# Optimization experiments

Hardware: AMD Instinct MI355X
Metric: run time of the kernel (lower is better)

Reference implementation:

```python
import jax, jax.numpy as jnp
import numpy as np

EPS = 1e-8
N_CLASSES = 11


def _instance_loss(views_1, views_2, masks, labels):
    # views_*: [1, C, H, W]; masks: [1, K, H, W] binary; labels: [1, K] in [0,11)
    C = views_1.shape[1]
    X1 = views_1[0].reshape(C, -1)                      # [C, P]
    X2 = views_2[0].reshape(C, -1)                      # [C, P]
    K = masks.shape[1]
    M = (masks[0].reshape(K, -1) == 1).astype(X1.dtype) # [K, P]
    lab = labels[0]                                     # [K]

    counts = M.sum(axis=1)                              # [K] pixels per instance
    cnt = jnp.maximum(counts, 1.0)

    # per-instance mean feature vector over masked view-1 pixels
    per_chan_sum = M @ X1.T                             # [K, C]
    means = per_chan_sum / cnt[:, None]                 # [K, C]

    # torch.std over ALL elements of the gathered [N_k, C] block (unbiased)
    n_elem = counts * C                                 # [K]
    sum_all = per_chan_sum.sum(axis=1)                  # [K]
    mean_all = sum_all / jnp.maximum(n_elem, 1.0)
    sumsq = M @ (X1 * X1).sum(axis=0)                   # [K]
    var = (sumsq - n_elem * mean_all * mean_all) / jnp.maximum(n_elem - 1.0, 1.0)
    std = jnp.sqrt(jnp.maximum(var, 0.0))               # [K]

    # pairwise mean cosine sim: sim[i,j] = mean_{p in mask_j} cos(means[i], X2[:,p])
    norm_m = jnp.sqrt((means * means).sum(axis=1))      # [K]
    norm_2 = jnp.sqrt((X2 * X2).sum(axis=0))            # [P]
    D = means @ X2                                      # [K, P]
    ratio = D / jnp.maximum(norm_m[:, None] * norm_2[None, :], EPS)
    sim = (ratio @ M.T) / cnt[None, :]                  # [K, K]

    same = lab[:, None] == lab[None, :]
    eye = jnp.eye(K, dtype=bool)

    instance_sim = jnp.zeros(N_CLASSES, X1.dtype).at[lab].add(jnp.diagonal(sim))
    class_sim = jnp.zeros(N_CLASSES, X1.dtype).at[lab].add(
        jnp.where(same & ~eye, sim, 0.0).sum(axis=1))
    class_std = jnp.zeros(N_CLASSES, X1.dtype).at[lab].add(std)

    # negative-pair buckets: human={1,2}, 4wheel={3..8}, 2wheel={9,10}
    g_hum_4w = (lab >= 1) & (lab <= 8)                  # human or 4wheel
    g_4w_2w = (lab >= 3) & (lab <= 10)                  # 4wheel or 2wheel
    g_hum_2w = ((lab >= 1) & (lab <= 2)) | ((lab >= 9) & (lab <= 10))
    diff = ~same

    def neg_bucket(g):
        pair = diff & g[:, None] & g[None, :]
        c = pair.sum().astype(X1.dtype)
        s = jnp.where(pair, sim, 0.0).sum()
        return jnp.where(c > 1, s / c, s).reshape(1)

    neg_4w_hum = neg_bucket(g_hum_4w)
    neg_4w_2w = neg_bucket(g_4w_2w)
    neg_hum_2w = neg_bucket(g_hum_2w)

    class_counts = jnp.zeros(N_CLASSES, X1.dtype).at[lab].add(1.0)
    many = class_counts > 1
    instance_sim = jnp.where(many, instance_sim / jnp.maximum(class_counts, 1.0), instance_sim)
    class_sim = jnp.where(
        many, class_sim / jnp.maximum(class_counts * (class_counts - 1.0), 1.0), class_sim)
    class_std = jnp.where(many, class_std / jnp.maximum(class_counts, 1.0), class_std)

    return instance_sim, class_sim, neg_4w_hum, neg_4w_2w, neg_hum_2w, class_std


def setup_inputs() -> dict:
    key = jax.random.key(0)
    k1, k2, k3, k4 = jax.random.split(key, 4)
    views_1 = jax.random.normal(k1, (1, 64, 512, 512), dtype=jnp.float32)
    views_2 = jax.random.normal(k2, (1, 64, 512, 512), dtype=jnp.float32)
    masks = jax.random.randint(k3, (1, 16, 512, 512), 0, 2, dtype=jnp.int32)
    labels = jax.random.randint(k4, (1, 16), 0, 11, dtype=jnp.int32)
    return {"views_1": views_1, "views_2": views_2, "masks": masks, "labels": labels}


def reference(views_1, views_2, masks, labels):
    return _instance_loss(views_1, views_2, masks, labels)
```

## Files before the change

kernel.cpp:

```cpp
#include <hip/hip_runtime.h>

#define PIX 262144
#define CCH 64
#define KK  16

typedef __attribute__((ext_vector_type(8))) short short8;
typedef __attribute__((ext_vector_type(4))) float f32x4;

__device__ __forceinline__ unsigned short f2bf(float f) {
    unsigned u = __float_as_uint(f);
    return (unsigned short)((u + 0x7FFFu + ((u >> 16) & 1u)) >> 16);
}
__device__ __forceinline__ float bf2f(unsigned short h) {
    return __uint_as_float(((unsigned)h) << 16);
}

__global__ __launch_bounds__(256) void k1a_pack(
        const int* __restrict__ masks, unsigned short* __restrict__ packed,
        float* __restrict__ counts_s) {
    int t = blockIdx.x * 256 + threadIdx.x;
    int p = t * 2;
    unsigned m0 = 0, m1 = 0;
    #pragma unroll
    for (int k = 0; k < KK; ++k) {
        int2 mv = *(const int2*)(masks + (size_t)k * PIX + p);
        m0 |= (unsigned)(mv.x == 1) << k;
        m1 |= (unsigned)(mv.y == 1) << k;
    }
    packed[p]     = (unsigned short)m0;
    packed[p + 1] = (unsigned short)m1;

    __shared__ float wc[4][16];
    int wid = threadIdx.x >> 6, lane = threadIdx.x & 63;
    #pragma unroll
    for (int k = 0; k < KK; ++k) {
        unsigned long long b0 = __ballot((m0 >> k) & 1u);
        unsigned long long b1 = __ballot((m1 >> k) & 1u);
        if (lane == 0) wc[wid][k] = (float)(__popcll(b0) + __popcll(b1));
    }
    __syncthreads();
    if (threadIdx.x < 16) {
        int k = threadIdx.x;
        float s = wc[0][k] + wc[1][k] + wc[2][k] + wc[3][k];
        atomicAdd(counts_s + k * 32 + (blockIdx.x & 31), s);
    }
}

__global__ __launch_bounds__(256) void k1b_ynorm(
        const float* __restrict__ x2, float* __restrict__ yv) {
    int p = (blockIdx.x * 256 + threadIdx.x) * 4;
    float4 s = make_float4(0.f, 0.f, 0.f, 0.f);
    #pragma unroll 16
    for (int c = 0; c < CCH; ++c) {
        float4 v = *(const float4*)(x2 + (size_t)c * PIX + p);
        s.x = fmaf(v.x, v.x, s.x);
        s.y = fmaf(v.y, v.y, s.y);
        s.z = fmaf(v.z, v.z, s.z);
        s.w = fmaf(v.w, v.w, s.w);
    }
    float4 y;
    y.x = (s.x > 0.f) ? rsqrtf(s.x) : 0.f;
    y.y = (s.y > 0.f) ? rsqrtf(s.y) : 0.f;
    y.z = (s.z > 0.f) ? rsqrtf(s.z) : 0.f;
    y.w = (s.w > 0.f) ? rsqrtf(s.w) : 0.f;
    *(float4*)(yv + p) = y;
}

__device__ __forceinline__ float wred64(float v) {
    #pragma unroll
    for (int o = 32; o > 0; o >>= 1) v += __shfl_xor(v, o, 64);
    return v;
}

__global__ __launch_bounds__(256) void k2_mfma(
        const float* __restrict__ x1, const float* __restrict__ x2,
        const unsigned short* __restrict__ packed, const float* __restrict__ yv,
        float* __restrict__ psum_f, float* __restrict__ psumsq_f,
        float* __restrict__ G_f) {
    int b = blockIdx.x;
    bool typeB = (b >= 512);
    if (typeB) b -= 512;
    int lane = threadIdx.x & 63;
    int wv   = threadIdx.x >> 6;
    int quad = lane >> 4;
    int n    = lane & 15;
    int ch   = wv * 16 + n;
    int base = b * 512;

    const float* Xrow = (typeB ? x2 : x1) + (size_t)ch * PIX;

    f32x4 acc0 = {0.f, 0.f, 0.f, 0.f};
    f32x4 acc1 = {0.f, 0.f, 0.f, 0.f};
    const short ONE = (short)0x3F80;

    for (int cki = 0; cki < 16; ++cki) {
        int kof = base + cki * 32 + (quad << 3);
        int4 pk = *(const int4*)(packed + kof);
        float4 xa = *(const float4*)(Xrow + kof);
        float4 xb = *(const float4*)(Xrow + kof + 4);

        short8 af;
        af[0] = ((pk.x >> n) & 1)        ? ONE : (short)0;
        af[1] = ((pk.x >> (n + 16)) & 1) ? ONE : (short)0;
        af[2] = ((pk.y >> n) & 1)        ? ONE : (short)0;
        af[3] = ((pk.y >> (n + 16)) & 1) ? ONE : (short)0;
        af[4] = ((pk.z >> n) & 1)        ? ONE : (short)0;
        af[5] = ((pk.z >> (n + 16)) & 1) ? ONE : (short)0;
        af[6] = ((pk.w >> n) & 1)        ? ONE : (short)0;
        af[7] = ((pk.w >> (n + 16)) & 1) ? ONE : (short)0;

        float xs[8] = {xa.x, xa.y, xa.z, xa.w, xb.x, xb.y, xb.z, xb.w};
        if (typeB) {
            float4 ya = *(const float4*)(yv + kof);
            float4 yb = *(const float4*)(yv + kof + 4);
            float ys[8] = {ya.x, ya.y, ya.z, ya.w, yb.x, yb.y, yb.z, yb.w};
            #pragma unroll
            for (int j = 0; j < 8; ++j) xs[j] *= ys[j];
        }

        short8 bh, bl;
        #pragma unroll
        for (int j = 0; j < 8; ++j) {
            float v = xs[j];
            unsigned short h = f2bf(v);
            bh[j] = (short)h;
            bl[j] = (short)f2bf(v - bf2f(h));
        }
        acc0 = __builtin_amdgcn_mfma_f32_16x16x32_bf16(af, bh, acc0, 0, 0, 0);
        acc0 = __builtin_amdgcn_mfma_f32_16x16x32_bf16(af, bl, acc0, 0, 0, 0);

        if (!typeB) {
            short8 qh, ql;
            #pragma unroll
            for (int j = 0; j < 8; ++j) {
                float sq = xs[j] * xs[j];
                unsigned short h = f2bf(sq);
                qh[j] = (short)h;
                ql[j] = (short)f2bf(sq - bf2f(h));
            }
            acc1 = __builtin_amdgcn_mfma_f32_16x16x32_bf16(af, qh, acc1, 0, 0, 0);
            acc1 = __builtin_amdgcn_mfma_f32_16x16x32_bf16(af, ql, acc1, 0, 0, 0);
        }
    }

    int col = wv * 16 + n;
    #pragma unroll
    for (int r = 0; r < 4; ++r) {
        int row = quad * 4 + r;
        if (typeB) {
            atomicAdd(G_f + row * 64 + col, acc0[r]);
        } else {
            atomicAdd(psum_f + row * 64 + col, acc0[r]);
            atomicAdd(psumsq_f + row * 64 + col, acc1[r]);
        }
    }
}

__global__ __launch_bounds__(256) void k3_finalize(
        const int* __restrict__ labels, const float* __restrict__ counts_s,
        const float* __restrict__ psum_f, const float* __restrict__ psumsq_f,
        const float* __restrict__ G_f, float* __restrict__ out) {
    __shared__ float meansS[16][65];
    __shared__ float Gs[16][65];
    __shared__ float cntS[16], rawcS[16], nmS[16], stdS[16], rowS[16];
    __shared__ float ssq2[16][17];
    __shared__ float ssqS[16];
    __shared__ int   labS[16];
    __shared__ float simS[16][17];
    __shared__ float bred[4][6];
    int t = threadIdx.x;

    if (t < 16) {
        float s = 0.f;
        #pragma unroll 8
        for (int j = 0; j < 32; ++j) s += counts_s[t * 32 + j];
        rawcS[t] = s;
        cntS[t]  = fmaxf(s, 1.f);
        labS[t]  = labels[t];
    }
    {
        int k = t >> 4, seg = t & 15;
        const float4 v = *(const float4*)(psumsq_f + k * 64 + seg * 4);
        ssq2[k][seg] = v.x + v.y + v.z + v.w;
    }
    __syncthreads();
    if (t < 16) {
        float s = 0.f;
        #pragma unroll
        for (int seg = 0; seg < 16; ++seg) s += ssq2[t][seg];
        ssqS[t] = s;
    }
    for (int i = t; i < 1024; i += 256) {
        int k = i >> 6, c = i & 63;
        meansS[k][c] = psum_f[i] / cntS[k];
        Gs[k][c] = G_f[i];
    }
    __syncthreads();
    if (t < 16) {
        float s2 = 0.f, sm = 0.f;
        for (int c = 0; c < 64; ++c) {
            float m = meansS[t][c];
            s2 = fmaf(m, m, s2);
            sm += m;
        }
        nmS[t] = sqrtf(s2);
        float ne = rawcS[t] * 64.f;
        float ma = (sm * cntS[t]) / fmaxf(ne, 1.f);
        float var = (ssqS[t] - ne * ma * ma) / fmaxf(ne - 1.f, 1.f);
        stdS[t] = sqrtf(fmaxf(var, 0.f));
    }
    __syncthreads();
    {
        int i = t >> 4, j = t & 15;
        float d = 0.f;
        #pragma unroll 16
        for (int c = 0; c < 64; ++c) d = fmaf(meansS[i][c], Gs[j][c], d);
        simS[i][j] = d / (fmaxf(nmS[i], 1e-30f) * cntS[j]);
    }
    __syncthreads();
    if (t < 16) {
        float s = 0.f;
        int li = labS[t];
        for (int j = 0; j < 16; ++j)
            if (j != t && labS[j] == li) s += simS[t][j];
        rowS[t] = s;
    }
    float s0 = 0.f, s1 = 0.f, s2 = 0.f, c0 = 0.f, c1 = 0.f, c2 = 0.f;
    {
        int i = t >> 4, j = t & 15;
        int li = labS[i], lj = labS[j];
        if (li != lj) {
            float sv = simS[i][j];
            bool gi0 = li >= 1 && li <= 8,  gj0 = lj >= 1 && lj <= 8;
            bool gi1 = li >= 3 && li <= 10, gj1 = lj >= 3 && lj <= 10;
            bool gi2 = (li >= 1 && li <= 2) || (li >= 9 && li <= 10);
            bool gj2 = (lj >= 1 && lj <= 2) || (lj >= 9 && lj <= 10);
            if (gi0 && gj0) { s0 = sv; c0 = 1.f; }
            if (gi1 && gj1) { s1 = sv; c1 = 1.f; }
            if (gi2 && gj2) { s2 = sv; c2 = 1.f; }
        }
    }
    s0 = wred64(s0); s1 = wred64(s1); s2 = wred64(s2);
    c0 = wred64(c0); c1 = wred64(c1); c2 = wred64(c2);
    {
        int wid = t >> 6, lane = t & 63;
        if (lane == 0) {
            bred[wid][0] = s0; bred[wid][1] = s1; bred[wid][2] = s2;
            bred[wid][3] = c0; bred[wid][4] = c1; bred[wid][5] = c2;
        }
    }
    __syncthreads();
    if (t < 11) {
        float cc = 0.f, inst = 0.f, csim = 0.f, cstd = 0.f;
        for (int k = 0; k < 16; ++k) {
            if (labS[k] == t) {
                cc += 1.f;
                inst += simS[k][k];
                csim += rowS[k];
                cstd += stdS[k];
            }
        }
        if (cc > 1.f) {
            inst /= fmaxf(cc, 1.f);
            csim /= fmaxf(cc * (cc - 1.f), 1.f);
            cstd /= cc;
        }
        out[t]      = inst;
        out[11 + t] = csim;
        out[25 + t] = cstd;
    }
    if (t == 0) {
        float S0 = bred[0][0] + bred[1][0] + bred[2][0] + bred[3][0];
        float S1 = bred[0][1] + bred[1][1] + bred[2][1] + bred[3][1];
        float S2 = bred[0][2] + bred[1][2] + bred[2][2] + bred[3][2];
        float C0 = bred[0][3] + bred[1][3] + bred[2][3] + bred[3][3];
        float C1 = bred[0][4] + bred[1][4] + bred[2][4] + bred[3][4];
        float C2 = bred[0][5] + bred[1][5] + bred[2][5] + bred[3][5];
        out[22] = (C0 > 1.f) ? (S0 / C0) : S0;
        out[23] = (C1 > 1.f) ? (S1 / C1) : S1;
        out[24] = (C2 > 1.f) ? (S2 / C2) : S2;
    }
}

extern "C" void kernel_launch(void* const* d_in, const int* in_sizes, int n_in,
                              void* d_out, int out_size, void* d_ws, size_t ws_size,
                              hipStream_t stream) {
    const float* x1     = (const float*)d_in[0];
    const float* x2     = (const float*)d_in[1];
    const int*   masks  = (const int*)d_in[2];
    const int*   labels = (const int*)d_in[3];
    float* out = (float*)d_out;

    char* ws = (char*)d_ws;
    unsigned short* packed = (unsigned short*)ws;
    float* yv       = (float*)(ws + (size_t)PIX * 2);
    float* counts_s = (float*)(ws + (size_t)PIX * 6);
    float* psum_f   = counts_s + 512;
    float* psumsq_f = psum_f + 1024;
    float* G_f      = psumsq_f + 1024;

    hipMemsetAsync(counts_s, 0, (512 + 3 * 1024) * sizeof(float), stream);
    k1a_pack<<<512, 256, 0, stream>>>(masks, packed, counts_s);
    k1b_ynorm<<<256, 256, 0, stream>>>(x2, yv);
    k2_mfma<<<1024, 256, 0, stream>>>(x1, x2, packed, yv, psum_f, psumsq_f, G_f);
    k3_finalize<<<1, 256, 0, stream>>>(labels, counts_s, psum_f, psumsq_f, G_f, out);
}
```

Before: 202.6 us.

## Fuse prep kernels, split main MFMA grid finer, and spread atomic accumulators

```diff
diff --git a/kernel.cpp b/kernel.cpp
--- a/kernel.cpp
+++ b/kernel.cpp
@@ -7,63 +7,52 @@
 typedef __attribute__((ext_vector_type(8))) short short8;
 typedef __attribute__((ext_vector_type(4))) float f32x4;
 
-__device__ __forceinline__ unsigned short f2bf(float f) {
-    unsigned u = __float_as_uint(f);
-    return (unsigned short)((u + 0x7FFFu + ((u >> 16) & 1u)) >> 16);
-}
-__device__ __forceinline__ float bf2f(unsigned short h) {
-    return __uint_as_float(((unsigned)h) << 16);
-}
-
-__global__ __launch_bounds__(256) void k1a_pack(
-        const int* __restrict__ masks, unsigned short* __restrict__ packed,
-        float* __restrict__ counts_s) {
-    int t = blockIdx.x * 256 + threadIdx.x;
-    int p = t * 2;
-    unsigned m0 = 0, m1 = 0;
-    #pragma unroll
-    for (int k = 0; k < KK; ++k) {
-        int2 mv = *(const int2*)(masks + (size_t)k * PIX + p);
-        m0 |= (unsigned)(mv.x == 1) << k;
-        m1 |= (unsigned)(mv.y == 1) << k;
-    }
-    packed[p]     = (unsigned short)m0;
-    packed[p + 1] = (unsigned short)m1;
-
+__global__ __launch_bounds__(256) void k1_fused(
+        const int* __restrict__ masks, const float* __restrict__ x2,
+        unsigned short* __restrict__ packed, float* __restrict__ counts_s,
+        float* __restrict__ yv) {
     __shared__ float wc[4][16];
-    int wid = threadIdx.x >> 6, lane = threadIdx.x & 63;
-    #pragma unroll
-    for (int k = 0; k < KK; ++k) {
-        unsigned long long b0 = __ballot((m0 >> k) & 1u);
-        unsigned long long b1 = __ballot((m1 >> k) & 1u);
-        if (lane == 0) wc[wid][k] = (float)(__popcll(b0) + __popcll(b1));
-    }
-    __syncthreads();
-    if (threadIdx.x < 16) {
-        int k = threadIdx.x;
-        float s = wc[0][k] + wc[1][k] + wc[2][k] + wc[3][k];
-        atomicAdd(counts_s + k * 32 + (blockIdx.x & 31), s);
-    }
-}
-
-__global__ __launch_bounds__(256) void k1b_ynorm(
-        const float* __restrict__ x2, float* __restrict__ yv) {
-    int p = (blockIdx.x * 256 + threadIdx.x) * 4;
-    float4 s = make_float4(0.f, 0.f, 0.f, 0.f);
-    #pragma unroll 16
-    for (int c = 0; c < CCH; ++c) {
-        float4 v = *(const float4*)(x2 + (size_t)c * PIX + p);
-        s.x = fmaf(v.x, v.x, s.x);
-        s.y = fmaf(v.y, v.y, s.y);
-        s.z = fmaf(v.z, v.z, s.z);
-        s.w = fmaf(v.w, v.w, s.w);
-    }
-    float4 y;
-    y.x = (s.x > 0.f) ? rsqrtf(s.x) : 0.f;
-    y.y = (s.y > 0.f) ? rsqrtf(s.y) : 0.f;
-    y.z = (s.z > 0.f) ? rsqrtf(s.z) : 0.f;
-    y.w = (s.w > 0.f) ? rsqrtf(s.w) : 0.f;
-    *(float4*)(yv + p) = y;
+    if (blockIdx.x < 512) {
+        int t = blockIdx.x * 256 + threadIdx.x;
+        int p = t * 2;
+        unsigned m0 = 0, m1 = 0;
+        #pragma unroll
+        for (int k = 0; k < KK; ++k) {
+            int2 mv = *(const int2*)(masks + (size_t)k * PIX + p);
+            m0 |= (unsigned)(mv.x == 1) << k;
+            m1 |= (unsigned)(mv.y == 1) << k;
+        }
+        packed[p]     = (unsigned short)m0;
+        packed[p + 1] = (unsigned short)m1;
+
+        int wid = threadIdx.x >> 6, lane = threadIdx.x & 63;
+        #pragma unroll
+        for (int k = 0; k < KK; ++k) {
+            unsigned long long b0 = __ballot((m0 >> k) & 1u);
+            unsigned long long b1 = __ballot((m1 >> k) & 1u);
+            if (lane == 0) wc[wid][k] = (float)(__popcll(b0) + __popcll(b1));
+        }
+        __syncthreads();
+        if (threadIdx.x < 16) {
+            int k = threadIdx.x;
+            float s = wc[0][k] + wc[1][k] + wc[2][k] + wc[3][k];
+            atomicAdd(counts_s + k * 32 + (blockIdx.x & 31), s);
+        }
+    } else {
+        int b2 = blockIdx.x - 512;
+        int p = (b2 * 256 + threadIdx.x) * 2;
+        float s0 = 0.f, s1 = 0.f;
+        #pragma unroll 16
+        for (int c = 0; c < CCH; ++c) {
+            float2 v = *(const float2*)(x2 + (size_t)c * PIX + p);
+            s0 = fmaf(v.x, v.x, s0);
+            s1 = fmaf(v.y, v.y, s1);
+        }
+        float2 y;
+        y.x = (s0 > 0.f) ? rsqrtf(s0) : 0.f;
+        y.y = (s1 > 0.f) ? rsqrtf(s1) : 0.f;
+        *(float2*)(yv + p) = y;
+    }
 }
 
 __device__ __forceinline__ float wred64(float v) {
@@ -75,45 +64,59 @@
 __global__ __launch_bounds__(256) void k2_mfma(
         const float* __restrict__ x1, const float* __restrict__ x2,
         const unsigned short* __restrict__ packed, const float* __restrict__ yv,
-        float* __restrict__ psum_f, float* __restrict__ psumsq_f,
-        float* __restrict__ G_f) {
+        float* __restrict__ psum_c, float* __restrict__ psumsq_c,
+        float* __restrict__ G_c) {
     int b = blockIdx.x;
-    bool typeB = (b >= 512);
-    if (typeB) b -= 512;
+    bool TB = (b >= 2048);
+    if (TB) b -= 2048;
     int lane = threadIdx.x & 63;
     int wv   = threadIdx.x >> 6;
     int quad = lane >> 4;
     int n    = lane & 15;
     int ch   = wv * 16 + n;
-    int base = b * 512;
-
-    const float* Xrow = (typeB ? x2 : x1) + (size_t)ch * PIX;
+    int base = b * 128;
+    int cp   = b & 31;
+
+    const float* Xrow = (TB ? x2 : x1) + (size_t)ch * PIX;
+
+    int4 pk[4]; float4 xa[4], xb[4], ya[4], yb[4];
+    #pragma unroll
+    for (int i = 0; i < 4; ++i) {
+        int kof = base + i * 32 + (quad << 3);
+        pk[i] = *(const int4*)(packed + kof);
+        xa[i] = *(const float4*)(Xrow + kof);
+        xb[i] = *(const float4*)(Xrow + kof + 4);
+    }
+    if (TB) {
+        #pragma unroll
+        for (int i = 0; i < 4; ++i) {
+            int kof = base + i * 32 + (quad << 3);
+            ya[i] = *(const float4*)(yv + kof);
+            yb[i] = *(const float4*)(yv + kof + 4);
+        }
+    }
 
     f32x4 acc0 = {0.f, 0.f, 0.f, 0.f};
     f32x4 acc1 = {0.f, 0.f, 0.f, 0.f};
     const short ONE = (short)0x3F80;
 
-    for (int cki = 0; cki < 16; ++cki) {
-        int kof = base + cki * 32 + (quad << 3);
-        int4 pk = *(const int4*)(packed + kof);
-        float4 xa = *(const float4*)(Xrow + kof);
-        float4 xb = *(const float4*)(Xrow + kof + 4);
-
+    #pragma unroll
+    for (int i = 0; i < 4; ++i) {
         short8 af;
-        af[0] = ((pk.x >> n) & 1)        ? ONE : (short)0;
-        af[1] = ((pk.x >> (n + 16)) & 1) ? ONE : (short)0;
-        af[2] = ((pk.y >> n) & 1)        ? ONE : (short)0;
-        af[3] = ((pk.y >> (n + 16)) & 1) ? ONE : (short)0;
-        af[4] = ((pk.z >> n) & 1)        ? ONE : (short)0;
-        af[5] = ((pk.z >> (n + 16)) & 1) ? ONE : (short)0;
-        af[6] = ((pk.w >> n) & 1)        ? ONE : (short)0;
-        af[7] = ((pk.w >> (n + 16)) & 1) ? ONE : (short)0;
-
-        float xs[8] = {xa.x, xa.y, xa.z, xa.w, xb.x, xb.y, xb.z, xb.w};
-        if (typeB) {
-            float4 ya = *(const float4*)(yv + kof);
-            float4 yb = *(const float4*)(yv + kof + 4);
-            float ys[8] = {ya.x, ya.y, ya.z, ya.w, yb.x, yb.y, yb.z, yb.w};
+        af[0] = ((pk[i].x >> n) & 1)        ? ONE : (short)0;
+        af[1] = ((pk[i].x >> (n + 16)) & 1) ? ONE : (short)0;
+        af[2] = ((pk[i].y >> n) & 1)        ? ONE : (short)0;
+        af[3] = ((pk[i].y >> (n + 16)) & 1) ? ONE : (short)0;
+        af[4] = ((pk[i].z >> n) & 1)        ? ONE : (short)0;
+        af[5] = ((pk[i].z >> (n + 16)) & 1) ? ONE : (short)0;
+        af[6] = ((pk[i].w >> n) & 1)        ? ONE : (short)0;
+        af[7] = ((pk[i].w >> (n + 16)) & 1) ? ONE : (short)0;
+
+        float xs[8] = {xa[i].x, xa[i].y, xa[i].z, xa[i].w,
+                       xb[i].x, xb[i].y, xb[i].z, xb[i].w};
+        if (TB) {
+            float ys[8] = {ya[i].x, ya[i].y, ya[i].z, ya[i].w,
+                           yb[i].x, yb[i].y, yb[i].z, yb[i].w};
             #pragma unroll
             for (int j = 0; j < 8; ++j) xs[j] *= ys[j];
         }
@@ -121,22 +124,23 @@
         short8 bh, bl;
         #pragma unroll
         for (int j = 0; j < 8; ++j) {
-            float v = xs[j];
-            unsigned short h = f2bf(v);
-            bh[j] = (short)h;
-            bl[j] = (short)f2bf(v - bf2f(h));
+            unsigned u = __float_as_uint(xs[j]);
+            bh[j] = (short)(u >> 16);
+            float hi = __uint_as_float(u & 0xFFFF0000u);
+            bl[j] = (short)(__float_as_uint(xs[j] - hi) >> 16);
         }
         acc0 = __builtin_amdgcn_mfma_f32_16x16x32_bf16(af, bh, acc0, 0, 0, 0);
         acc0 = __builtin_amdgcn_mfma_f32_16x16x32_bf16(af, bl, acc0, 0, 0, 0);
 
-        if (!typeB) {
+        if (!TB) {
             short8 qh, ql;
             #pragma unroll
             for (int j = 0; j < 8; ++j) {
                 float sq = xs[j] * xs[j];
-                unsigned short h = f2bf(sq);
-                qh[j] = (short)h;
-                ql[j] = (short)f2bf(sq - bf2f(h));
+                unsigned u = __float_as_uint(sq);
+                qh[j] = (short)(u >> 16);
+                float hi = __uint_as_float(u & 0xFFFF0000u);
+                ql[j] = (short)(__float_as_uint(sq - hi) >> 16);
             }
             acc1 = __builtin_amdgcn_mfma_f32_16x16x32_bf16(af, qh, acc1, 0, 0, 0);
             acc1 = __builtin_amdgcn_mfma_f32_16x16x32_bf16(af, ql, acc1, 0, 0, 0);
@@ -146,20 +150,20 @@
     int col = wv * 16 + n;
     #pragma unroll
     for (int r = 0; r < 4; ++r) {
-        int row = quad * 4 + r;
-        if (typeB) {
-            atomicAdd(G_f + row * 64 + col, acc0[r]);
+        int idx = cp * 1024 + (quad * 4 + r) * 64 + col;
+        if (TB) {
+            atomicAdd(G_c + idx, acc0[r]);
         } else {
-            atomicAdd(psum_f + row * 64 + col, acc0[r]);
-            atomicAdd(psumsq_f + row * 64 + col, acc1[r]);
+            atomicAdd(psum_c + idx, acc0[r]);
+            atomicAdd(psumsq_c + idx, acc1[r]);
         }
     }
 }
 
 __global__ __launch_bounds__(256) void k3_finalize(
         const int* __restrict__ labels, const float* __restrict__ counts_s,
-        const float* __restrict__ psum_f, const float* __restrict__ psumsq_f,
-        const float* __restrict__ G_f, float* __restrict__ out) {
+        const float* __restrict__ psum_c, const float* __restrict__ psumsq_c,
+        const float* __restrict__ G_c, float* __restrict__ out) {
     __shared__ float meansS[16][65];
     __shared__ float Gs[16][65];
     __shared__ float cntS[16], rawcS[16], nmS[16], stdS[16], rowS[16];
@@ -180,8 +184,12 @@
     }
     {
         int k = t >> 4, seg = t & 15;
-        const float4 v = *(const float4*)(psumsq_f + k * 64 + seg * 4);
-        ssq2[k][seg] = v.x + v.y + v.z + v.w;
+        float s = 0.f;
+        for (int cp = 0; cp < 32; ++cp) {
+            const float4 v = *(const float4*)(psumsq_c + cp * 1024 + k * 64 + seg * 4);
+            s += v.x + v.y + v.z + v.w;
+        }
+        ssq2[k][seg] = s;
     }
     __syncthreads();
     if (t < 16) {
@@ -192,8 +200,14 @@
     }
     for (int i = t; i < 1024; i += 256) {
         int k = i >> 6, c = i & 63;
-        meansS[k][c] = psum_f[i] / cntS[k];
-        Gs[k][c] = G_f[i];
+        float sp = 0.f, sg = 0.f;
+        #pragma unroll 8
+        for (int cp = 0; cp < 32; ++cp) {
+            sp += psum_c[cp * 1024 + i];
+            sg += G_c[cp * 1024 + i];
+        }
+        meansS[k][c] = sp / cntS[k];
+        Gs[k][c] = sg;
     }
     __syncthreads();
     if (t < 16) {
@@ -295,13 +309,12 @@
     unsigned short* packed = (unsigned short*)ws;
     float* yv       = (float*)(ws + (size_t)PIX * 2);
     float* counts_s = (float*)(ws + (size_t)PIX * 6);
-    float* psum_f   = counts_s + 512;
-    float* psumsq_f = psum_f + 1024;
-    float* G_f      = psumsq_f + 1024;
-
-    hipMemsetAsync(counts_s, 0, (512 + 3 * 1024) * sizeof(float), stream);
-    k1a_pack<<<512, 256, 0, stream>>>(masks, packed, counts_s);
-    k1b_ynorm<<<256, 256, 0, stream>>>(x2, yv);
-    k2_mfma<<<1024, 256, 0, stream>>>(x1, x2, packed, yv, psum_f, psumsq_f, G_f);
-    k3_finalize<<<1, 256, 0, stream>>>(labels, counts_s, psum_f, psumsq_f, G_f, out);
-}
+    float* psum_c   = counts_s + 512;
+    float* psumsq_c = psum_c + 32 * 1024;
+    float* G_c      = psumsq_c + 32 * 1024;
+
+    hipMemsetAsync(counts_s, 0, (512 + 3 * 32 * 1024) * sizeof(float), stream);
+    k1_fused<<<1024, 256, 0, stream>>>(masks, x2, packed, counts_s, yv);
+    k2_mfma<<<4096, 256, 0, stream>>>(x1, x2, packed, yv, psum_c, psumsq_c, G_c);
+    k3_finalize<<<1, 256, 0, stream>>>(labels, counts_s, psum_c, psumsq_c, G_c, out);
+}
```

Result: no change. 202.0 us (-0.3%).
